# Kernel optimization log

Measured on AMD Instinct MI355X. Metric: run time of the kernel, lower is better.

## Reference

```python
import jax, jax.numpy as jnp
import numpy as np

TEMP = 0.07
LAMBDA_CON = 1.0
LAMBDA_SHELL = 1.0
NEG_INF = -1e30


def setup_inputs() -> dict:
    key = jax.random.key(0)
    k1, k2, k3, k4, k5 = jax.random.split(key, 5)
    B, D = 8192, 1024
    emb = jax.random.normal(k1, (B, D), jnp.float32)
    emb = emb / jnp.linalg.norm(emb, axis=1, keepdims=True)  # encoder outputs are unit-norm
    center = jax.random.normal(k2, (D,), jnp.float32)
    center = center / jnp.linalg.norm(center)  # buffer is F.normalize'd in estimate_epoch_geometry
    labels = jax.random.randint(k3, (B,), 0, 2)  # 0 = machine, 1 = human
    radius_m = jax.random.uniform(k4, (1,), jnp.float32)
    radius_h = radius_m + jax.random.uniform(k5, (1,), jnp.float32)  # radius_h >= radius_m by construction
    return {"embeddings": emb, "center": center, "radius_m": radius_m,
            "radius_h": radius_h, "labels": labels}


def reference(embeddings, center, radius_m, radius_h, labels):
    rm = radius_m[0]
    rh = radius_h[0]
    B = embeddings.shape[0]

    # ---- shell loss ----
    distances = jnp.linalg.norm(embeddings - center[None, :], axis=1)  # [B]
    mmask = labels == 0
    hmask = labels == 1
    nm = jnp.sum(mmask)
    nh = jnp.sum(hmask)
    loss_m = jnp.sum(jnp.where(mmask, jnp.square(jax.nn.relu(distances - rm)), 0.0)) / jnp.maximum(nm, 1)
    loss_h = jnp.sum(jnp.where(hmask, jnp.square(jax.nn.relu(rh - distances)), 0.0)) / jnp.maximum(nh, 1)
    loss_shell = loss_m + loss_h

    # ---- contrastive loss (batched: one BxB sim matrix instead of per-anchor loop) ----
    S = (embeddings @ embeddings.T) / TEMP          # [B, B] pairwise logits
    Sp = (embeddings @ center) / TEMP               # [B]  logits vs prototype
    eye = jnp.eye(B, dtype=bool)
    S_masked = jnp.where(eye, jnp.asarray(NEG_INF, S.dtype), S)
    # denominator per machine anchor i: logsumexp over {other machines, prototype, humans}
    # (labels are only 0/1, so all j != i contribute) plus the prototype logit
    lse = jnp.logaddexp(jax.nn.logsumexp(S_masked, axis=1), Sp)  # [B]
    # positives for machine anchor i: other machines (nm-1) + prototype -> nm positives
    pos_sum = jnp.sum(jnp.where(mmask[None, :] & ~eye, S, 0.0), axis=1) + Sp  # [B]
    anchor_loss = lse - pos_sum / jnp.maximum(nm, 1)
    con_sum = jnp.sum(jnp.where(mmask, anchor_loss, 0.0))
    # prototype as anchor: positives = machines, negatives = humans
    lse_p = jax.nn.logsumexp(Sp)
    proto_loss = lse_p - jnp.sum(jnp.where(mmask, Sp, 0.0)) / jnp.maximum(nm, 1)
    loss_con = (con_sum + proto_loss) / jnp.maximum(nm + 1, 1)
    # original returns 0 when either class is empty
    both = (nm > 0) & (nh > 0)
    loss_con = jnp.where(both, loss_con, 0.0)

    loss = LAMBDA_SHELL * loss_shell + LAMBDA_CON * loss_con
    return (loss, loss_shell, loss_m, loss_h, loss_con, distances)
```

## Files before the change

kernel.cpp:

```cpp
#include <hip/hip_runtime.h>

#define INV_T 14.285714285714286f
#define C1 0.055803571428571425f

typedef float f32x16 __attribute__((ext_vector_type(16)));
typedef float f32x4 __attribute__((ext_vector_type(4)));
typedef int i32x4v __attribute__((ext_vector_type(4)));
typedef int i32x8 __attribute__((ext_vector_type(8)));

__device__ __forceinline__ unsigned char f2e4m3(float f) {
    unsigned char s = (unsigned char)((__float_as_uint(f) >> 24) & 0x80);
    float a = fabsf(f);
    if (a > 448.f) a = 448.f;
    if (a == 0.f) return s;
    int e = (int)((__float_as_uint(a) >> 23) & 0xFF) - 127;
    if (e < -10) return s;
    if (e < -6) e = -6;
    float scale = __int_as_float((unsigned)(130 - e) << 23);
    int mi = (int)rintf(a * scale);
    if (mi >= 16) { mi >>= 1; ++e; }
    if (mi < 8) return s | (unsigned char)mi;
    return s | (unsigned char)(((e + 7) << 3) | (mi - 8));
}

__device__ __forceinline__ void async16(void* l, const void* g) {
    __builtin_amdgcn_global_load_lds(
        (const __attribute__((address_space(1))) unsigned int*)g,
        (__attribute__((address_space(3))) unsigned int*)l, 16, 0, 0);
}

__global__ void __launch_bounds__(256) k_prep(const float* __restrict__ emb,
                                              const float* __restrict__ center,
                                              unsigned char* __restrict__ embQ,
                                              float* __restrict__ out,
                                              float* __restrict__ Sp, int D, int B) {
    int tid = threadIdx.x;
    int wave = tid >> 6, lane = tid & 63;
    int gw = blockIdx.x * 4 + wave;
    int nw = gridDim.x * 4;
    const float4* c4 = (const float4*)center;
    for (int i = gw; i < B; i += nw) {
        const float4* row = (const float4*)(emb + (size_t)i * D);
        uchar4* qrow = embQ ? (uchar4*)(embQ + (size_t)i * D) : nullptr;
        float d2 = 0.f, sp = 0.f;
#pragma unroll
        for (int j = 0; j < 4; ++j) {
            int idx = lane + j * 64;
            float4 e = row[idx];
            float4 c = c4[idx];
            float dx = e.x - c.x, dy = e.y - c.y, dz = e.z - c.z, dw = e.w - c.w;
            d2 += dx * dx + dy * dy + dz * dz + dw * dw;
            sp += e.x * c.x + e.y * c.y + e.z * c.z + e.w * c.w;
            if (qrow)
                qrow[idx] = make_uchar4(f2e4m3(e.x * 16.f), f2e4m3(e.y * 16.f),
                                        f2e4m3(e.z * 16.f), f2e4m3(e.w * 16.f));
        }
#pragma unroll
        for (int m = 1; m <= 32; m <<= 1) {
            d2 += __shfl_xor(d2, m, 64);
            sp += __shfl_xor(sp, m, 64);
        }
        if (lane == 0) {
            out[5 + i] = sqrtf(d2);
            Sp[i] = sp * INV_T;
        }
    }
}

__global__ void __launch_bounds__(256) k_colsum(const float* __restrict__ emb,
                                                const int* __restrict__ labels,
                                                float* __restrict__ s_m,
                                                int* __restrict__ cnt, int D) {
    int t = threadIdx.x;
    int r0 = blockIdx.x * 32;
    float4 acc = {0.f, 0.f, 0.f, 0.f};
#pragma unroll 4
    for (int r = 0; r < 32; ++r) {
        float sc = (labels[r0 + r] == 0) ? 1.f : 0.f;
        float4 v = ((const float4*)(emb + (size_t)(r0 + r) * D))[t];
        acc.x += v.x * sc; acc.y += v.y * sc; acc.z += v.z * sc; acc.w += v.w * sc;
    }
    atomicAdd(&s_m[t * 4 + 0], acc.x);
    atomicAdd(&s_m[t * 4 + 1], acc.y);
    atomicAdd(&s_m[t * 4 + 2], acc.z);
    atomicAdd(&s_m[t * 4 + 3], acc.w);
    if (t == 0) {
        int c = 0;
        for (int r = 0; r < 32; ++r) c += (labels[r0 + r] == 0) ? 1 : 0;
        atomicAdd(cnt, c);
    }
}

#define MXMFMA(a, b, c) __builtin_amdgcn_mfma_scale_f32_32x32x64_f8f6f4( \
    (a), (b), (c), 0, 0, 0, 0x7F7F7F7F, 0, 0x7F7F7F7F)

__global__ void __launch_bounds__(256, 2)
k_sumexp_mx(const unsigned char* __restrict__ embQ, float* __restrict__ sumexp,
            int D, int nT) {
    int bid = blockIdx.x;
    const int n = nT;
    float nf = (float)n + 0.5f;
    int rb = (int)(nf - sqrtf(fmaxf(nf * nf - 2.0f * (float)bid, 0.f)));
    if (rb < 0) rb = 0;
    if (rb > n - 1) rb = n - 1;
#define TRI_OFF(r) ((r) * n - ((r) * ((r)-1)) / 2)
    while (rb + 1 <= n - 1 && TRI_OFF(rb + 1) <= bid) ++rb;
    while (rb > 0 && TRI_OFF(rb) > bid) --rb;
    int cb = rb + (bid - TRI_OFF(rb));
#undef TRI_OFF
    int rowbase = rb * 128, colbase = cb * 128;

    int tid = threadIdx.x;
    int wave = tid >> 6, lane = tid & 63;
    int wr = wave >> 1, wc = wave & 1;
    int l31 = lane & 31, kk = lane >> 5;

    __shared__ unsigned char sA[2][16384];
    __shared__ unsigned char sB[2][16384];
    __shared__ float rred[2][128];
    __shared__ float cred[2][128];

    f32x16 acc[2][2];
#pragma unroll
    for (int fr = 0; fr < 2; ++fr)
#pragma unroll
        for (int fc = 0; fc < 2; ++fc)
#pragma unroll
            for (int v = 0; v < 16; ++v) acc[fr][fc][v] = 0.f;

    const int kG = D >> 7;

    const unsigned char* gSA[4];
    const unsigned char* gSB[4];
    unsigned int dstOff[4];
#pragma unroll
    for (int q = 0; q < 4; ++q) {
        int ch = q * 256 + tid;
        int row = ch >> 3, lc = ch & 7;
        int gc = lc ^ (row & 7);
        gSA[q] = embQ + (size_t)(rowbase + row) * D + gc * 16;
        gSB[q] = embQ + (size_t)(colbase + row) * D + gc * 16;
        dstOff[q] = (unsigned)ch << 4;
    }

    auto stage = [&](int buf, int kt) {
        int ko = kt << 7;
#pragma unroll
        for (int q = 0; q < 4; ++q) {
            async16(&sA[buf][dstOff[q]], gSA[q] + ko);
            async16(&sB[buf][dstOff[q]], gSB[q] + ko);
        }
    };

    int e7 = (l31 & 7) << 4;
    int offs[2][2];
#pragma unroll
    for (int h = 0; h < 2; ++h)
#pragma unroll
        for (int j = 0; j < 2; ++j)
            offs[h][j] = (((h * 4 + kk * 2 + j) << 4) ^ e7);
    int aBase0 = (wr * 64 + l31) << 7;
    int aBase1 = aBase0 + (32 << 7);
    int bBase0 = (wc * 64 + l31) << 7;
    int bBase1 = bBase0 + (32 << 7);

    stage(0, 0);
    for (int kt = 0; kt < kG; ++kt) {
        int cur = kt & 1;
        __syncthreads();
        if (kt + 1 < kG) stage(cur ^ 1, kt + 1);
        const unsigned char* A = sA[cur];
        const unsigned char* Bp = sB[cur];
#pragma unroll
        for (int h = 0; h < 2; ++h) {
            i32x8 av[2], bv[2];
            {
                i32x4v lo = *(const i32x4v*)&A[aBase0 + offs[h][0]];
                i32x4v hi = *(const i32x4v*)&A[aBase0 + offs[h][1]];
                av[0] = __builtin_shufflevector(lo, hi, 0, 1, 2, 3, 4, 5, 6, 7);
            }
            {
                i32x4v lo = *(const i32x4v*)&A[aBase1 + offs[h][0]];
                i32x4v hi = *(const i32x4v*)&A[aBase1 + offs[h][1]];
                av[1] = __builtin_shufflevector(lo, hi, 0, 1, 2, 3, 4, 5, 6, 7);
            }
            {
                i32x4v lo = *(const i32x4v*)&Bp[bBase0 + offs[h][0]];
                i32x4v hi = *(const i32x4v*)&Bp[bBase0 + offs[h][1]];
                bv[0] = __builtin_shufflevector(lo, hi, 0, 1, 2, 3, 4, 5, 6, 7);
            }
            {
                i32x4v lo = *(const i32x4v*)&Bp[bBase1 + offs[h][0]];
                i32x4v hi = *(const i32x4v*)&Bp[bBase1 + offs[h][1]];
                bv[1] = __builtin_shufflevector(lo, hi, 0, 1, 2, 3, 4, 5, 6, 7);
            }
#pragma unroll
            for (int fr = 0; fr < 2; ++fr)
#pragma unroll
                for (int fc = 0; fc < 2; ++fc)
                    acc[fr][fc] = MXMFMA(av[fr], bv[fc], acc[fr][fc]);
        }
    }

    float rs[2][16];
    float cs[2] = {0.f, 0.f};
#pragma unroll
    for (int fr = 0; fr < 2; ++fr)
#pragma unroll
        for (int v = 0; v < 16; ++v) rs[fr][v] = 0.f;

#pragma unroll
    for (int fr = 0; fr < 2; ++fr)
#pragma unroll
        for (int fc = 0; fc < 2; ++fc) {
            int gcol = colbase + wc * 64 + fc * 32 + l31;
#pragma unroll
            for (int v = 0; v < 16; ++v) {
                int grow = rowbase + wr * 64 + fr * 32 + (v & 3) + 8 * (v >> 2) + 4 * kk;
                float e = (grow < gcol) ? __expf(acc[fr][fc][v] * C1 - INV_T) : 0.f;
                rs[fr][v] += e;
                cs[fc] += e;
            }
        }

#pragma unroll
    for (int m = 1; m <= 16; m <<= 1)
#pragma unroll
        for (int fr = 0; fr < 2; ++fr)
#pragma unroll
            for (int v = 0; v < 16; ++v) rs[fr][v] += __shfl_xor(rs[fr][v], m, 64);
    if (l31 == 0)
#pragma unroll
        for (int fr = 0; fr < 2; ++fr)
#pragma unroll
            for (int v = 0; v < 16; ++v)
                rred[wc][wr * 64 + fr * 32 + (v & 3) + 8 * (v >> 2) + 4 * kk] = rs[fr][v];

#pragma unroll
    for (int fc = 0; fc < 2; ++fc) cs[fc] += __shfl_xor(cs[fc], 32, 64);
    if (kk == 0)
#pragma unroll
        for (int fc = 0; fc < 2; ++fc) cred[wr][wc * 64 + fc * 32 + l31] = cs[fc];

    __syncthreads();
    if (tid < 128) {
        atomicAdd(&sumexp[rowbase + tid], rred[0][tid] + rred[1][tid]);
    } else {
        int u = tid - 128;
        atomicAdd(&sumexp[colbase + u], cred[0][u] + cred[1][u]);
    }
}

typedef __bf16 bf16x8 __attribute__((ext_vector_type(8)));
typedef unsigned short u16x8 __attribute__((ext_vector_type(8)));
__device__ __forceinline__ unsigned short f2bf(float f) {
    unsigned int x = __float_as_uint(f);
    x += 0x7fffu + ((x >> 16) & 1u);
    return (unsigned short)(x >> 16);
}
__global__ void __launch_bounds__(256) k_sumexp_fb(const float* __restrict__ embF,
                                                   float* __restrict__ sumexp, int D, int nTiles) {
    int bid = blockIdx.x;
    const int n = nTiles;
    float nf = (float)n + 0.5f;
    int rb = (int)(nf - sqrtf(fmaxf(nf * nf - 2.0f * (float)bid, 0.f)));
    if (rb < 0) rb = 0;
    if (rb > n - 1) rb = n - 1;
#define TRI_OFF(r) ((r) * n - ((r) * ((r)-1)) / 2)
    while (rb + 1 <= n - 1 && TRI_OFF(rb + 1) <= bid) ++rb;
    while (rb > 0 && TRI_OFF(rb) > bid) --rb;
    int cb = rb + (bid - TRI_OFF(rb));
#undef TRI_OFF
    int tid = threadIdx.x;
    int wave = tid >> 6, lane = tid & 63;
    int wr = wave >> 1, wc = wave & 1;
    int quad = lane >> 4, l15 = lane & 15;
    int rowbase = rb * 128, colbase = cb * 128;
    __shared__ unsigned short lA[128 * 64];
    __shared__ unsigned short lB[128 * 64];
    __shared__ float rred[2][128];
    __shared__ float cred[2][128];
    f32x4 zero = {0.f, 0.f, 0.f, 0.f};
    f32x4 acc[4][4];
#pragma unroll
    for (int r = 0; r < 4; ++r)
#pragma unroll
        for (int c = 0; c < 4; ++c) acc[r][c] = zero;
    const int kIters = D >> 6;
    for (int kt = 0; kt < kIters; ++kt) {
        int k0 = kt << 6;
#pragma unroll
        for (int q = 0; q < 4; ++q) {
            int ch = q * 256 + tid;
            int row = ch >> 3, lc = ch & 7;
            int pc = lc ^ (row & 7);
            const float4* sa = (const float4*)(embF + (size_t)(rowbase + row) * D + k0 + lc * 8);
            const float4* sb = (const float4*)(embF + (size_t)(colbase + row) * D + k0 + lc * 8);
            float4 a0 = sa[0], a1 = sa[1];
            float4 b0 = sb[0], b1 = sb[1];
            u16x8 va = {f2bf(a0.x), f2bf(a0.y), f2bf(a0.z), f2bf(a0.w),
                        f2bf(a1.x), f2bf(a1.y), f2bf(a1.z), f2bf(a1.w)};
            u16x8 vb = {f2bf(b0.x), f2bf(b0.y), f2bf(b0.z), f2bf(b0.w),
                        f2bf(b1.x), f2bf(b1.y), f2bf(b1.z), f2bf(b1.w)};
            *(u16x8*)&lA[(row << 6) + (pc << 3)] = va;
            *(u16x8*)&lB[(row << 6) + (pc << 3)] = vb;
        }
        __syncthreads();
#pragma unroll
        for (int h = 0; h < 2; ++h) {
            bf16x8 af[4], bfr[4];
#pragma unroll
            for (int r = 0; r < 4; ++r) {
                int row = wr * 64 + r * 16 + l15;
                int pc = (h * 4 + quad) ^ (l15 & 7);
                af[r] = *(const bf16x8*)&lA[(row << 6) + (pc << 3)];
            }
#pragma unroll
            for (int c = 0; c < 4; ++c) {
                int row = wc * 64 + c * 16 + l15;
                int pc = (h * 4 + quad) ^ (l15 & 7);
                bfr[c] = *(const bf16x8*)&lB[(row << 6) + (pc << 3)];
            }
#pragma unroll
            for (int r = 0; r < 4; ++r)
#pragma unroll
                for (int c = 0; c < 4; ++c)
                    acc[r][c] = __builtin_amdgcn_mfma_f32_16x16x32_bf16(af[r], bfr[c], acc[r][c], 0, 0, 0);
        }
        __syncthreads();
    }
    float rs[4][4], cs[4];
#pragma unroll
    for (int r = 0; r < 4; ++r)
#pragma unroll
        for (int v = 0; v < 4; ++v) rs[r][v] = 0.f;
#pragma unroll
    for (int c = 0; c < 4; ++c) cs[c] = 0.f;
#pragma unroll
    for (int r = 0; r < 4; ++r)
#pragma unroll
        for (int c = 0; c < 4; ++c) {
            f32x4 a = acc[r][c];
            int gcol = colbase + wc * 64 + c * 16 + l15;
#pragma unroll
            for (int v = 0; v < 4; ++v) {
                int grow = rowbase + wr * 64 + r * 16 + quad * 4 + v;
                float e = (grow < gcol) ? __expf((a[v] - 1.0f) * INV_T) : 0.f;
                rs[r][v] += e;
                cs[c] += e;
            }
        }
#pragma unroll
    for (int m = 1; m <= 8; m <<= 1)
#pragma unroll
        for (int r = 0; r < 4; ++r)
#pragma unroll
            for (int v = 0; v < 4; ++v) rs[r][v] += __shfl_xor(rs[r][v], m, 64);
    if (l15 == 0)
#pragma unroll
        for (int r = 0; r < 4; ++r)
#pragma unroll
            for (int v = 0; v < 4; ++v)
                rred[wc][wr * 64 + r * 16 + quad * 4 + v] = rs[r][v];
#pragma unroll
    for (int m = 16; m <= 32; m <<= 1)
#pragma unroll
        for (int c = 0; c < 4; ++c) cs[c] += __shfl_xor(cs[c], m, 64);
    if (quad == 0)
#pragma unroll
        for (int c = 0; c < 4; ++c) cred[wr][wc * 64 + c * 16 + l15] = cs[c];
    __syncthreads();
    if (tid < 128) {
        atomicAdd(&sumexp[rowbase + tid], rred[0][tid] + rred[1][tid]);
    } else {
        int u = tid & 127;
        atomicAdd(&sumexp[colbase + u], cred[0][u] + cred[1][u]);
    }
}

__global__ void __launch_bounds__(256) k_finalize(const float* __restrict__ emb,
                                                  const float* __restrict__ s_m,
                                                  const float* __restrict__ Sp,
                                                  const float* __restrict__ sumexp,
                                                  const int* __restrict__ labels,
                                                  const float* __restrict__ outv,
                                                  const float* __restrict__ rmp,
                                                  const float* __restrict__ rhp,
                                                  float* __restrict__ scal, int D) {
    int tid = threadIdx.x;
    int wave = tid >> 6, lane = tid & 63;
    __shared__ float ac[8];
    if (tid < 8) ac[tid] = 0.f;
    __syncthreads();
    float rm = rmp[0], rh = rhp[0];
    const float4* sm4 = (const float4*)s_m;
    for (int it = 0; it < 8; ++it) {
        int i = blockIdx.x * 32 + it * 4 + wave;
        const float4* row = (const float4*)(emb + (size_t)i * D);
        float q = 0.f, sd = 0.f;
#pragma unroll
        for (int j = 0; j < 4; ++j) {
            int idx = lane + j * 64;
            float4 e = row[idx];
            float4 s = sm4[idx];
            q += e.x * s.x + e.y * s.y + e.z * s.z + e.w * s.w;
            sd += e.x * e.x + e.y * e.y + e.z * e.z + e.w * e.w;
        }
#pragma unroll
        for (int m = 1; m <= 32; m <<= 1) {
            q += __shfl_xor(q, m, 64);
            sd += __shfl_xor(sd, m, 64);
        }
        if (lane == 0) {
            float LP = Sp[i];
            float eS = __expf(LP - INV_T);
            float lse = INV_T + __logf(sumexp[i] + eS);
            bool mach = (labels[i] == 0);
            float pos = (q - (mach ? sd : 0.f)) * INV_T + LP;
            float d = outv[5 + i];
            atomicAdd(&ac[2], eS);
            if (mach) {
                atomicAdd(&ac[4], lse);
                atomicAdd(&ac[5], pos);
                atomicAdd(&ac[3], LP);
                float x = d - rm;
                if (x > 0.f) atomicAdd(&ac[0], x * x);
            } else {
                float x = rh - d;
                if (x > 0.f) atomicAdd(&ac[1], x * x);
            }
        }
    }
    __syncthreads();
    if (tid < 8) atomicAdd(&scal[tid], ac[tid]);
}

__global__ void k_final(const float* __restrict__ scal, const int* __restrict__ cnt,
                        float* __restrict__ out, int B) {
    if (threadIdx.x == 0) {
        int nm = cnt[0], nh = B - nm;
        float nmf = (float)(nm > 1 ? nm : 1);
        float nhf = (float)(nh > 1 ? nh : 1);
        float loss_m = scal[0] / nmf;
        float loss_h = scal[1] / nhf;
        float loss_shell = loss_m + loss_h;
        float lse_p = INV_T + __logf(scal[2]);
        float proto = lse_p - scal[3] / nmf;
        float con = scal[4] - scal[5] / nmf;
        int denom = (nm + 1 > 1) ? nm + 1 : 1;
        float lc = (con + proto) / (float)denom;
        if (!(nm > 0 && nh > 0)) lc = 0.f;
        out[0] = loss_shell + lc;
        out[1] = loss_shell;
        out[2] = loss_m;
        out[3] = loss_h;
        out[4] = lc;
    }
}

extern "C" void kernel_launch(void* const* d_in, const int* in_sizes, int n_in,
                              void* d_out, int out_size, void* d_ws, size_t ws_size,
                              hipStream_t stream) {
    const float* emb = (const float*)d_in[0];
    const float* center = (const float*)d_in[1];
    const float* rmp = (const float*)d_in[2];
    const float* rhp = (const float*)d_in[3];
    const int* labels = (const int*)d_in[4];
    float* out = (float*)d_out;
    const int B = in_sizes[4];
    const int D = in_sizes[1];

    size_t qBytes = (size_t)B * D;
    size_t auxBytes = (size_t)B * 4 + (size_t)D * 4 + 256 + (size_t)B * 4;
    bool pre = ws_size >= qBytes + auxBytes;
    size_t Z0 = pre ? qBytes : 0;

    char* ws = (char*)d_ws;
    unsigned char* embQ = (unsigned char*)ws;
    float* sumexp = (float*)(ws + Z0);
    float* s_m = (float*)(ws + Z0 + (size_t)B * 4);
    float* scal = (float*)(ws + Z0 + (size_t)B * 4 + (size_t)D * 4);
    int* cnt = (int*)(scal + 8);
    float* Sp = (float*)(ws + Z0 + (size_t)B * 4 + (size_t)D * 4 + 256);

    hipMemsetAsync(ws + Z0, 0, (size_t)B * 4 + (size_t)D * 4 + 256, stream);

    k_prep<<<512, 256, 0, stream>>>(emb, center, pre ? embQ : nullptr, out, Sp, D, B);
    k_colsum<<<B / 32, D / 4, 0, stream>>>(emb, labels, s_m, cnt, D);

    int nT = B / 128;
    int nBlocks = nT * (nT + 1) / 2;
    if (pre) k_sumexp_mx<<<nBlocks, 256, 0, stream>>>(embQ, sumexp, D, nT);
    else     k_sumexp_fb<<<nBlocks, 256, 0, stream>>>(emb, sumexp, D, nT);

    k_finalize<<<B / 32, 256, 0, stream>>>(emb, s_m, Sp, sumexp, labels, out, rmp, rhp, scal, D);
    k_final<<<1, 64, 0, stream>>>(scal, cnt, out, B);
}
```

Baseline: 199.8 us.

## Use triple-buffered K=64 stages with vmcnt waits in sumexp GEMM

The FP8 MX GEMM main loop now uses three 8KB shared-memory stages of K=64 instead of two 16KB stages of K=128. It prefetches two stages ahead and waits on outstanding loads with explicit s_waitcnt vmcnt plus a bare barrier instead of __syncthreads. It also raises occupancy to 3 blocks per CU, uses a new swizzled layout that packs two rows per 128-byte line, and raises wave priority around the MFMAs. The goal is to hide global-load latency better and fit more blocks per CU. The cost is twice as many barriers per K, and the manual vmcnt counting is fragile.

```diff
diff --git a/kernel.cpp b/kernel.cpp
--- a/kernel.cpp
+++ b/kernel.cpp
@@ -94,7 +94,7 @@
 #define MXMFMA(a, b, c) __builtin_amdgcn_mfma_scale_f32_32x32x64_f8f6f4( \
     (a), (b), (c), 0, 0, 0, 0x7F7F7F7F, 0, 0x7F7F7F7F)
 
-__global__ void __launch_bounds__(256, 2)
+__global__ void __launch_bounds__(256, 3)
 k_sumexp_mx(const unsigned char* __restrict__ embQ, float* __restrict__ sumexp,
             int D, int nT) {
     int bid = blockIdx.x;
@@ -115,8 +115,8 @@
     int wr = wave >> 1, wc = wave & 1;
     int l31 = lane & 31, kk = lane >> 5;
 
-    __shared__ unsigned char sA[2][16384];
-    __shared__ unsigned char sB[2][16384];
+    __shared__ unsigned char sA[3][8192];
+    __shared__ unsigned char sB[3][8192];
     __shared__ float rred[2][128];
     __shared__ float cred[2][128];
 
@@ -128,78 +128,82 @@
 #pragma unroll
             for (int v = 0; v < 16; ++v) acc[fr][fc][v] = 0.f;
 
-    const int kG = D >> 7;
-
-    const unsigned char* gSA[4];
-    const unsigned char* gSB[4];
-    unsigned int dstOff[4];
-#pragma unroll
-    for (int q = 0; q < 4; ++q) {
+    const int kG = D >> 6;
+
+    const unsigned char* gA[2];
+    const unsigned char* gB[2];
+    unsigned int dstOff[2];
+#pragma unroll
+    for (int q = 0; q < 2; ++q) {
         int ch = q * 256 + tid;
-        int row = ch >> 3, lc = ch & 7;
-        int gc = lc ^ (row & 7);
-        gSA[q] = embQ + (size_t)(rowbase + row) * D + gc * 16;
-        gSB[q] = embQ + (size_t)(colbase + row) * D + gc * 16;
+        int L = ch >> 3;
+        int t = ch & 7;
+        int u = t ^ (L & 7);
+        int row = (L << 1) | (u >> 2);
+        int s = u & 3;
+        gA[q] = embQ + (size_t)(rowbase + row) * D + s * 16;
+        gB[q] = embQ + (size_t)(colbase + row) * D + s * 16;
         dstOff[q] = (unsigned)ch << 4;
     }
 
     auto stage = [&](int buf, int kt) {
-        int ko = kt << 7;
-#pragma unroll
-        for (int q = 0; q < 4; ++q) {
-            async16(&sA[buf][dstOff[q]], gSA[q] + ko);
-            async16(&sB[buf][dstOff[q]], gSB[q] + ko);
-        }
+        int ko = kt << 6;
+        async16(&sA[buf][dstOff[0]], gA[0] + ko);
+        async16(&sA[buf][dstOff[1]], gA[1] + ko);
+        async16(&sB[buf][dstOff[0]], gB[0] + ko);
+        async16(&sB[buf][dstOff[1]], gB[1] + ko);
     };
 
-    int e7 = (l31 & 7) << 4;
-    int offs[2][2];
-#pragma unroll
-    for (int h = 0; h < 2; ++h)
-#pragma unroll
-        for (int j = 0; j < 2; ++j)
-            offs[h][j] = (((h * 4 + kk * 2 + j) << 4) ^ e7);
-    int aBase0 = (wr * 64 + l31) << 7;
-    int aBase1 = aBase0 + (32 << 7);
-    int bBase0 = (wc * 64 + l31) << 7;
-    int bBase1 = bBase0 + (32 << 7);
+    int aOff[2][2], bOff[2][2];
+#pragma unroll
+    for (int f = 0; f < 2; ++f) {
+        int ra = wr * 64 + f * 32 + l31;
+        int La = ra >> 1, ha = (ra & 1) << 2, wa = La & 7;
+        int rbv = wc * 64 + f * 32 + l31;
+        int Lb = rbv >> 1, hb = (rbv & 1) << 2, wb = Lb & 7;
+#pragma unroll
+        for (int j = 0; j < 2; ++j) {
+            aOff[f][j] = (La << 7) + (((ha | (kk * 2 + j)) ^ wa) << 4);
+            bOff[f][j] = (Lb << 7) + (((hb | (kk * 2 + j)) ^ wb) << 4);
+        }
+    }
 
     stage(0, 0);
+    if (kG > 1) stage(1, 1);
+
+    int cur = 0;
     for (int kt = 0; kt < kG; ++kt) {
-        int cur = kt & 1;
-        __syncthreads();
-        if (kt + 1 < kG) stage(cur ^ 1, kt + 1);
+        if (kt + 1 < kG) {
+            asm volatile("s_waitcnt vmcnt(4)" ::: "memory");
+        } else {
+            asm volatile("s_waitcnt vmcnt(0)" ::: "memory");
+        }
+        __builtin_amdgcn_s_barrier();
+        if (kt + 2 < kG) {
+            int nxt = cur + 2;
+            if (nxt >= 3) nxt -= 3;
+            stage(nxt, kt + 2);
+        }
         const unsigned char* A = sA[cur];
         const unsigned char* Bp = sB[cur];
-#pragma unroll
-        for (int h = 0; h < 2; ++h) {
-            i32x8 av[2], bv[2];
-            {
-                i32x4v lo = *(const i32x4v*)&A[aBase0 + offs[h][0]];
-                i32x4v hi = *(const i32x4v*)&A[aBase0 + offs[h][1]];
-                av[0] = __builtin_shufflevector(lo, hi, 0, 1, 2, 3, 4, 5, 6, 7);
-            }
-            {
-                i32x4v lo = *(const i32x4v*)&A[aBase1 + offs[h][0]];
-                i32x4v hi = *(const i32x4v*)&A[aBase1 + offs[h][1]];
-                av[1] = __builtin_shufflevector(lo, hi, 0, 1, 2, 3, 4, 5, 6, 7);
-            }
-            {
-                i32x4v lo = *(const i32x4v*)&Bp[bBase0 + offs[h][0]];
-                i32x4v hi = *(const i32x4v*)&Bp[bBase0 + offs[h][1]];
-                bv[0] = __builtin_shufflevector(lo, hi, 0, 1, 2, 3, 4, 5, 6, 7);
-            }
-            {
-                i32x4v lo = *(const i32x4v*)&Bp[bBase1 + offs[h][0]];
-                i32x4v hi = *(const i32x4v*)&Bp[bBase1 + offs[h][1]];
-                bv[1] = __builtin_shufflevector(lo, hi, 0, 1, 2, 3, 4, 5, 6, 7);
-            }
-#pragma unroll
-            for (int fr = 0; fr < 2; ++fr)
-#pragma unroll
-                for (int fc = 0; fc < 2; ++fc)
-                    acc[fr][fc] = MXMFMA(av[fr], bv[fc], acc[fr][fc]);
-        }
+        i32x8 av[2], bv[2];
+#pragma unroll
+        for (int f = 0; f < 2; ++f) {
+            i32x4v lo = *(const i32x4v*)&A[aOff[f][0]];
+            i32x4v hi = *(const i32x4v*)&A[aOff[f][1]];
+            av[f] = __builtin_shufflevector(lo, hi, 0, 1, 2, 3, 4, 5, 6, 7);
+            i32x4v lo2 = *(const i32x4v*)&Bp[bOff[f][0]];
+            i32x4v hi2 = *(const i32x4v*)&Bp[bOff[f][1]];
+            bv[f] = __builtin_shufflevector(lo2, hi2, 0, 1, 2, 3, 4, 5, 6, 7);
+        }
+        __builtin_amdgcn_s_setprio(1);
+#pragma unroll
+        for (int fr = 0; fr < 2; ++fr)
+#pragma unroll
+            for (int fc = 0; fc < 2; ++fc)
+                acc[fr][fc] = MXMFMA(av[fr], bv[fc], acc[fr][fc]);
+        __builtin_amdgcn_s_setprio(0);
+        if (++cur == 3) cur = 0;
     }
 
     float rs[2][16];
```

After: 195.8 us. 2.0% less time.

## Fuse prep with column sum, fold final into finalize, remap GEMM blocks for XCDs

Applied to the files above, without the earlier changes.

Merges the prep kernel (distances, prototype logits, FP8 quantization) with the machine column-sum kernel so embeddings are read once. Folds the single-thread final kernel into finalize using a last-block-done counter with fences. Remaps triangular tile block IDs so consecutive tiles land on the same XCD, aiming for better L2 reuse. Together these cut launches and an extra full read of the embeddings, at the cost of a cross-block reduction through shared memory and an atomic completion counter.

```diff
diff --git a/kernel.cpp b/kernel.cpp
--- a/kernel.cpp
+++ b/kernel.cpp
@@ -29,66 +29,57 @@
         (__attribute__((address_space(3))) unsigned int*)l, 16, 0, 0);
 }
 
-__global__ void __launch_bounds__(256) k_prep(const float* __restrict__ emb,
-                                              const float* __restrict__ center,
-                                              unsigned char* __restrict__ embQ,
-                                              float* __restrict__ out,
-                                              float* __restrict__ Sp, int D, int B) {
-    int tid = threadIdx.x;
-    int wave = tid >> 6, lane = tid & 63;
-    int gw = blockIdx.x * 4 + wave;
-    int nw = gridDim.x * 4;
-    const float4* c4 = (const float4*)center;
-    for (int i = gw; i < B; i += nw) {
-        const float4* row = (const float4*)(emb + (size_t)i * D);
-        uchar4* qrow = embQ ? (uchar4*)(embQ + (size_t)i * D) : nullptr;
-        float d2 = 0.f, sp = 0.f;
-#pragma unroll
-        for (int j = 0; j < 4; ++j) {
-            int idx = lane + j * 64;
-            float4 e = row[idx];
-            float4 c = c4[idx];
-            float dx = e.x - c.x, dy = e.y - c.y, dz = e.z - c.z, dw = e.w - c.w;
-            d2 += dx * dx + dy * dy + dz * dz + dw * dw;
-            sp += e.x * c.x + e.y * c.y + e.z * c.z + e.w * c.w;
-            if (qrow)
-                qrow[idx] = make_uchar4(f2e4m3(e.x * 16.f), f2e4m3(e.y * 16.f),
-                                        f2e4m3(e.z * 16.f), f2e4m3(e.w * 16.f));
-        }
+__global__ void __launch_bounds__(256) k_prepcs(const float* __restrict__ emb,
+                                                const float* __restrict__ center,
+                                                const int* __restrict__ labels,
+                                                unsigned char* __restrict__ embQ,
+                                                float* __restrict__ out,
+                                                float* __restrict__ Sp,
+                                                float* __restrict__ s_m,
+                                                int* __restrict__ cnt, int D) {
+    int t = threadIdx.x;
+    int wave = t >> 6, lane = t & 63;
+    int nw = blockDim.x >> 6;
+    int r0 = blockIdx.x * 16;
+    __shared__ float redD[16][8];
+    __shared__ float redS[16][8];
+    float4 c = ((const float4*)center)[t];
+    float4 colacc = {0.f, 0.f, 0.f, 0.f};
+    int mcount = 0;
+    for (int r = 0; r < 16; ++r) {
+        int row = r0 + r;
+        int lab = labels[row];
+        float sc = (lab == 0) ? 1.f : 0.f;
+        mcount += (lab == 0) ? 1 : 0;
+        float4 e = ((const float4*)(emb + (size_t)row * D))[t];
+        float dx = e.x - c.x, dy = e.y - c.y, dz = e.z - c.z, dw = e.w - c.w;
+        float d2 = dx * dx + dy * dy + dz * dz + dw * dw;
+        float sp = e.x * c.x + e.y * c.y + e.z * c.z + e.w * c.w;
+        colacc.x += e.x * sc; colacc.y += e.y * sc;
+        colacc.z += e.z * sc; colacc.w += e.w * sc;
+        if (embQ)
+            ((uchar4*)(embQ + (size_t)row * D))[t] =
+                make_uchar4(f2e4m3(e.x * 16.f), f2e4m3(e.y * 16.f),
+                            f2e4m3(e.z * 16.f), f2e4m3(e.w * 16.f));
 #pragma unroll
         for (int m = 1; m <= 32; m <<= 1) {
             d2 += __shfl_xor(d2, m, 64);
             sp += __shfl_xor(sp, m, 64);
         }
-        if (lane == 0) {
-            out[5 + i] = sqrtf(d2);
-            Sp[i] = sp * INV_T;
-        }
-    }
-}
-
-__global__ void __launch_bounds__(256) k_colsum(const float* __restrict__ emb,
-                                                const int* __restrict__ labels,
-                                                float* __restrict__ s_m,
-                                                int* __restrict__ cnt, int D) {
-    int t = threadIdx.x;
-    int r0 = blockIdx.x * 32;
-    float4 acc = {0.f, 0.f, 0.f, 0.f};
-#pragma unroll 4
-    for (int r = 0; r < 32; ++r) {
-        float sc = (labels[r0 + r] == 0) ? 1.f : 0.f;
-        float4 v = ((const float4*)(emb + (size_t)(r0 + r) * D))[t];
-        acc.x += v.x * sc; acc.y += v.y * sc; acc.z += v.z * sc; acc.w += v.w * sc;
-    }
-    atomicAdd(&s_m[t * 4 + 0], acc.x);
-    atomicAdd(&s_m[t * 4 + 1], acc.y);
-    atomicAdd(&s_m[t * 4 + 2], acc.z);
-    atomicAdd(&s_m[t * 4 + 3], acc.w);
-    if (t == 0) {
-        int c = 0;
-        for (int r = 0; r < 32; ++r) c += (labels[r0 + r] == 0) ? 1 : 0;
-        atomicAdd(cnt, c);
-    }
+        if (lane == 0) { redD[r][wave] = d2; redS[r][wave] = sp; }
+    }
+    atomicAdd(&s_m[t * 4 + 0], colacc.x);
+    atomicAdd(&s_m[t * 4 + 1], colacc.y);
+    atomicAdd(&s_m[t * 4 + 2], colacc.z);
+    atomicAdd(&s_m[t * 4 + 3], colacc.w);
+    __syncthreads();
+    if (t < 16) {
+        float d2 = 0.f, sp = 0.f;
+        for (int w = 0; w < nw; ++w) { d2 += redD[t][w]; sp += redS[t][w]; }
+        out[5 + r0 + t] = sqrtf(d2);
+        Sp[r0 + t] = sp * INV_T;
+    }
+    if (t == 0) atomicAdd(cnt, mcount);
 }
 
 #define MXMFMA(a, b, c) __builtin_amdgcn_mfma_scale_f32_32x32x64_f8f6f4( \
@@ -97,8 +88,13 @@
 __global__ void __launch_bounds__(256, 2)
 k_sumexp_mx(const unsigned char* __restrict__ embQ, float* __restrict__ sumexp,
             int D, int nT) {
+    const int n = nT;
+    int nwg = n * (n + 1) / 2;
     int bid = blockIdx.x;
-    const int n = nT;
+    if ((nwg & 7) == 0) {
+        int cpx = nwg >> 3;
+        bid = (bid & 7) * cpx + (bid >> 3);
+    }
     float nf = (float)n + 0.5f;
     int rb = (int)(nf - sqrtf(fmaxf(nf * nf - 2.0f * (float)bid, 0.f)));
     if (rb < 0) rb = 0;
@@ -386,7 +382,11 @@
                                                   const float* __restrict__ outv,
                                                   const float* __restrict__ rmp,
                                                   const float* __restrict__ rhp,
-                                                  float* __restrict__ scal, int D) {
+                                                  float* __restrict__ scal,
+                                                  int* __restrict__ cnt,
+                                                  unsigned* __restrict__ done_ctr,
+                                                  float* __restrict__ out,
+                                                  int D, int B) {
     int tid = threadIdx.x;
     int wave = tid >> 6, lane = tid & 63;
     __shared__ float ac[8];
@@ -433,28 +433,34 @@
     }
     __syncthreads();
     if (tid < 8) atomicAdd(&scal[tid], ac[tid]);
-}
-
-__global__ void k_final(const float* __restrict__ scal, const int* __restrict__ cnt,
-                        float* __restrict__ out, int B) {
-    if (threadIdx.x == 0) {
-        int nm = cnt[0], nh = B - nm;
-        float nmf = (float)(nm > 1 ? nm : 1);
-        float nhf = (float)(nh > 1 ? nh : 1);
-        float loss_m = scal[0] / nmf;
-        float loss_h = scal[1] / nhf;
-        float loss_shell = loss_m + loss_h;
-        float lse_p = INV_T + __logf(scal[2]);
-        float proto = lse_p - scal[3] / nmf;
-        float con = scal[4] - scal[5] / nmf;
-        int denom = (nm + 1 > 1) ? nm + 1 : 1;
-        float lc = (con + proto) / (float)denom;
-        if (!(nm > 0 && nh > 0)) lc = 0.f;
-        out[0] = loss_shell + lc;
-        out[1] = loss_shell;
-        out[2] = loss_m;
-        out[3] = loss_h;
-        out[4] = lc;
+    __syncthreads();
+    if (tid == 0) {
+        __threadfence();
+        unsigned done = atomicAdd(done_ctr, 1u);
+        if (done == (unsigned)gridDim.x - 1) {
+            __threadfence();
+            float s[8];
+#pragma unroll
+            for (int i = 0; i < 8; ++i) s[i] = atomicAdd(&scal[i], 0.f);
+            int nm = atomicAdd(cnt, 0);
+            int nh = B - nm;
+            float nmf = (float)(nm > 1 ? nm : 1);
+            float nhf = (float)(nh > 1 ? nh : 1);
+            float loss_m = s[0] / nmf;
+            float loss_h = s[1] / nhf;
+            float loss_shell = loss_m + loss_h;
+            float lse_p = INV_T + __logf(s[2]);
+            float proto = lse_p - s[3] / nmf;
+            float con = s[4] - s[5] / nmf;
+            int denom = (nm + 1 > 1) ? nm + 1 : 1;
+            float lc = (con + proto) / (float)denom;
+            if (!(nm > 0 && nh > 0)) lc = 0.f;
+            out[0] = loss_shell + lc;
+            out[1] = loss_shell;
+            out[2] = loss_m;
+            out[3] = loss_h;
+            out[4] = lc;
+        }
     }
 }
 
@@ -472,7 +478,7 @@
 
     size_t qBytes = (size_t)B * D;
     size_t auxBytes = (size_t)B * 4 + (size_t)D * 4 + 256 + (size_t)B * 4;
-    bool pre = ws_size >= qBytes + auxBytes;
+    bool pre = (ws_size >= qBytes + auxBytes) && (B % 128 == 0) && (D % 128 == 0);
     size_t Z0 = pre ? qBytes : 0;
 
     char* ws = (char*)d_ws;
@@ -481,18 +487,19 @@
     float* s_m = (float*)(ws + Z0 + (size_t)B * 4);
     float* scal = (float*)(ws + Z0 + (size_t)B * 4 + (size_t)D * 4);
     int* cnt = (int*)(scal + 8);
+    unsigned* done_ctr = (unsigned*)(cnt + 1);
     float* Sp = (float*)(ws + Z0 + (size_t)B * 4 + (size_t)D * 4 + 256);
 
     hipMemsetAsync(ws + Z0, 0, (size_t)B * 4 + (size_t)D * 4 + 256, stream);
 
-    k_prep<<<512, 256, 0, stream>>>(emb, center, pre ? embQ : nullptr, out, Sp, D, B);
-    k_colsum<<<B / 32, D / 4, 0, stream>>>(emb, labels, s_m, cnt, D);
+    k_prepcs<<<B / 16, D / 4, 0, stream>>>(emb, center, labels,
+                                           pre ? embQ : nullptr, out, Sp, s_m, cnt, D);
 
     int nT = B / 128;
     int nBlocks = nT * (nT + 1) / 2;
     if (pre) k_sumexp_mx<<<nBlocks, 256, 0, stream>>>(embQ, sumexp, D, nT);
     else     k_sumexp_fb<<<nBlocks, 256, 0, stream>>>(emb, sumexp, D, nT);
 
-    k_finalize<<<B / 32, 256, 0, stream>>>(emb, s_m, Sp, sumexp, labels, out, rmp, rhp, scal, D);
-    k_final<<<1, 64, 0, stream>>>(scal, cnt, out, B);
-}
+    k_finalize<<<B / 32, 256, 0, stream>>>(emb, s_m, Sp, sumexp, labels, out,
+                                           rmp, rhp, scal, cnt, done_ctr, out, D, B);
+}
```

Result: slower. 229.4 us (+14.8%).
